# Kernel optimization log

Measured on AMD Instinct MI355X. Metric: run time of the kernel, lower is better.

## Reference

```python
import jax, jax.numpy as jnp
import numpy as np
from jax import lax

NUM_ITERS = 3
EPSILON = 0.5
QUEUE = 32768
NUM_CLUSTER = 1000


def setup_inputs() -> dict:
    key = jax.random.key(0)
    k1, _ = jax.random.split(key)
    memory_logits = jax.random.normal(k1, (QUEUE, NUM_CLUSTER), dtype=jnp.float32)
    learn_k = jnp.ones((1,), dtype=jnp.float32) * 5.0  # init value in torch module
    return {"memory_logits": memory_logits, "learn_k": learn_k}


def reference(memory_logits, learn_k):
    C = memory_logits.shape[1]
    # stabilize then exp, transpose to [C, N]
    ml = memory_logits - jnp.max(memory_logits)
    Q = jnp.exp(ml / EPSILON).T  # [C, N]
    # K: softmax over clusters of w * log(sigmoid(learn_k)); w = n/(C-1)
    w = (jnp.arange(C, dtype=Q.dtype) / (C - 1)).reshape(1, -1)
    K = jax.nn.softmax(w * jnp.log(jax.nn.sigmoid(learn_k)), axis=1)  # [1, C]
    Kcol = K.reshape(-1, 1)  # [C, 1] for row-wise scaling of Q
    B = Q.shape[1]
    # sort rows by descending row-sum
    order = jnp.argsort(-jnp.sum(Q, axis=1))
    Q = Q[order]
    Q = Q / jnp.sum(Q)

    def body(Q, _):
        Q = Q / jnp.sum(Q, axis=1, keepdims=True)   # row normalize
        Q = Q * Kcol                                 # (Q.t() * K).t()
        Q = jnp.clip(Q, 1e-16, None)
        Q = Q / jnp.sum(Q, axis=0, keepdims=True)   # col normalize
        Q = Q / B
        return Q, None

    Q, _ = lax.scan(body, Q, None, length=NUM_ITERS)
    Q = Q * B
    reorder = jnp.argsort(order)
    Q = Q[reorder]
    return Q.T  # [N, C]
```

## Files before the change

kernel.cpp:

```cpp
#include <hip/hip_runtime.h>
#include <math.h>

#define NQ 32768
#define NC 1000
#define NC4 250
#define NB 1024
#define PSTRIDE 1024

__device__ __forceinline__ float wredsum(float v) {
#pragma unroll
    for (int off = 32; off > 0; off >>= 1) v += __shfl_xor(v, off, 64);
    return v;
}

template <int MODE>
__global__ __launch_bounds__(256) void k_pass(const float* __restrict__ in,
                                              const float* __restrict__ svec,
                                              float* __restrict__ outp) {
    __shared__ float sacc[NC];
    if (MODE < 2) {
        for (int i = threadIdx.x; i < NC; i += 256) sacc[i] = 0.f;
        __syncthreads();
    }
    const int lane = threadIdx.x & 63;
    const int nw = (gridDim.x * 256) >> 6;
    const int wave = (blockIdx.x * 256 + threadIdx.x) >> 6;

    float4 sf[4];
    if (MODE >= 1) {
        const float4* S4 = reinterpret_cast<const float4*>(svec);
#pragma unroll
        for (int k = 0; k < 4; ++k) {
            int c4 = k * 64 + lane;
            sf[k] = (c4 < NC4) ? S4[c4] : make_float4(0.f, 0.f, 0.f, 0.f);
        }
    }
    float acc[16];
    if (MODE < 2) {
#pragma unroll
        for (int i = 0; i < 16; ++i) acc[i] = 0.f;
    }

    float4 nxt[4];
#pragma unroll
    for (int k = 0; k < 4; ++k) nxt[k] = make_float4(0.f, 0.f, 0.f, 0.f);

    int row = wave;
    if (row < NQ) {
        const float4* rp = reinterpret_cast<const float4*>(in + (size_t)row * NC);
#pragma unroll
        for (int k = 0; k < 4; ++k) {
            int c4 = k * 64 + lane;
            if (c4 < NC4) nxt[k] = rp[c4];
        }
    }
    while (row < NQ) {
        float4 cur[4];
#pragma unroll
        for (int k = 0; k < 4; ++k) cur[k] = nxt[k];
        const int nrow = row + nw;
        if (nrow < NQ) {
            const float4* rp = reinterpret_cast<const float4*>(in + (size_t)nrow * NC);
#pragma unroll
            for (int k = 0; k < 4; ++k) {
                int c4 = k * 64 + lane;
                if (c4 < NC4) nxt[k] = rp[c4];
            }
        }
        float4 e[4];
#pragma unroll
        for (int k = 0; k < 4; ++k) {
            e[k].x = __expf(2.f * cur[k].x);
            e[k].y = __expf(2.f * cur[k].y);
            e[k].z = __expf(2.f * cur[k].z);
            e[k].w = __expf(2.f * cur[k].w);
        }
        if (MODE == 0) {
#pragma unroll
            for (int k = 0; k < 4; ++k) {
                acc[4 * k + 0] += e[k].x; acc[4 * k + 1] += e[k].y;
                acc[4 * k + 2] += e[k].z; acc[4 * k + 3] += e[k].w;
            }
        } else {
            float t = 0.f;
#pragma unroll
            for (int k = 0; k < 4; ++k) {
                t += e[k].x * sf[k].x + e[k].y * sf[k].y
                   + e[k].z * sf[k].z + e[k].w * sf[k].w;
            }
            t = wredsum(t);
            const float r = 1.0f / t;
            if (MODE == 1) {
#pragma unroll
                for (int k = 0; k < 4; ++k) {
                    acc[4 * k + 0] += e[k].x * r; acc[4 * k + 1] += e[k].y * r;
                    acc[4 * k + 2] += e[k].z * r; acc[4 * k + 3] += e[k].w * r;
                }
            } else {
                float4* op = reinterpret_cast<float4*>(outp + (size_t)row * NC);
#pragma unroll
                for (int k = 0; k < 4; ++k) {
                    int c4 = k * 64 + lane;
                    if (c4 < NC4) {
                        op[c4] = make_float4(e[k].x * sf[k].x * r,
                                             e[k].y * sf[k].y * r,
                                             e[k].z * sf[k].z * r,
                                             e[k].w * sf[k].w * r);
                    }
                }
            }
        }
        row = nrow;
    }
    if (MODE < 2) {
#pragma unroll
        for (int k = 0; k < 4; ++k) {
            int c4 = k * 64 + lane;
            if (c4 < NC4) {
                atomicAdd(&sacc[4 * c4 + 0], acc[4 * k + 0]);
                atomicAdd(&sacc[4 * c4 + 1], acc[4 * k + 1]);
                atomicAdd(&sacc[4 * c4 + 2], acc[4 * k + 2]);
                atomicAdd(&sacc[4 * c4 + 3], acc[4 * k + 3]);
            }
        }
        __syncthreads();
        float* prow = outp + (size_t)blockIdx.x * PSTRIDE;
        for (int i = threadIdx.x; i < NC; i += 256) prow[i] = sacc[i];
    }
}

__global__ __launch_bounds__(128) void k_reduceG(const float* __restrict__ part,
                                                 float* __restrict__ G) {
    const int c = (blockIdx.x & 7) * 128 + threadIdx.x;
    const int p0 = (blockIdx.x >> 3) * 256;
    if (c < NC) {
        float sum = 0.f;
        for (int p = p0; p < p0 + 256; p += 4) {
            sum += part[(size_t)p * PSTRIDE + c]
                 + part[(size_t)(p + 1) * PSTRIDE + c]
                 + part[(size_t)(p + 2) * PSTRIDE + c]
                 + part[(size_t)(p + 3) * PSTRIDE + c];
        }
        atomicAdd(&G[c], sum);
    }
}

__global__ __launch_bounds__(128) void k_rank(const float* __restrict__ G,
                                              const float* __restrict__ learn_k,
                                              float* __restrict__ Ksc,
                                              float* __restrict__ svec) {
    __shared__ float sS[NC];
    __shared__ float sred[2];
    for (int i = threadIdx.x; i < NC; i += 128) sS[i] = G[i];
    const float L = -log1pf(expf(-learn_k[0]));
    float part = 0.f;
    for (int i = threadIdx.x; i < NC; i += 128)
        part += expf((float)i * (1.0f / 999.0f) * L);
    part = wredsum(part);
    if ((threadIdx.x & 63) == 0) sred[threadIdx.x >> 6] = part;
    __syncthreads();
    const float denom = sred[0] + sred[1];
    const int c = blockIdx.x * 128 + threadIdx.x;
    if (c < NC) {
        const float sc = sS[c];
        int p = 0;
#pragma unroll 4
        for (int j = 0; j < NC; ++j) {
            float sj = sS[j];
            p += (sj > sc) || (sj == sc && j < c);
        }
        const float ks = expf((float)p * (1.0f / 999.0f) * L) / denom;
        Ksc[c] = ks;
        svec[c] = ks / sc;
    }
}

__global__ __launch_bounds__(256) void k_prepS(const float* __restrict__ Ksc,
                                               const float* __restrict__ G,
                                               float* __restrict__ svec) {
    const int i = blockIdx.x * 256 + threadIdx.x;
    if (i < NC) svec[i] = Ksc[i] / G[i];
}

extern "C" void kernel_launch(void* const* d_in, const int* in_sizes, int n_in,
                              void* d_out, int out_size, void* d_ws, size_t ws_size,
                              hipStream_t stream) {
    const float* A = (const float*)d_in[0];
    const float* lk = (const float*)d_in[1];
    float* out = (float*)d_out;
    float* ws = (float*)d_ws;
    float* G0 = ws;
    float* G1 = ws + 1024;
    float* G2 = ws + 2048;
    float* Ksc = ws + 3072;
    float* sv = ws + 4096;
    float* part = ws + 8192;

    hipMemsetAsync(ws, 0, 3072 * sizeof(float), stream);

    k_pass<0><<<NB, 256, 0, stream>>>(A, nullptr, part);
    k_reduceG<<<32, 128, 0, stream>>>(part, G0);
    k_rank<<<8, 128, 0, stream>>>(G0, lk, Ksc, sv);
    k_pass<1><<<NB, 256, 0, stream>>>(A, sv, part);
    k_reduceG<<<32, 128, 0, stream>>>(part, G1);
    k_prepS<<<4, 256, 0, stream>>>(Ksc, G1, sv);
    k_pass<1><<<NB, 256, 0, stream>>>(A, sv, part);
    k_reduceG<<<32, 128, 0, stream>>>(part, G2);
    k_prepS<<<4, 256, 0, stream>>>(Ksc, G2, sv);
    k_pass<2><<<NB, 256, 0, stream>>>(A, sv, out);
}
```

Measured before the change: 451.1 us.

## Fuse all Sinkhorn passes into one cooperative persistent kernel with grid sync

Replaces the ten-launch pipeline (four streaming passes, partial-sum reductions, rank and scale kernels) with a single cooperative kernel. Column sums are accumulated into global arrays through shared-memory and global atomics, and the phases are separated by grid.sync. Rank and scale computation is repeated redundantly in every block's shared memory, and rows are streamed in chunks of 8 contiguous rows per wave. This removes launch gaps and the partial-buffer round trip, at the cost of grid-wide barriers, a grid capped by occupancy, and global atomic contention.

```diff
diff --git a/kernel.cpp b/kernel.cpp
--- a/kernel.cpp
+++ b/kernel.cpp
@@ -1,11 +1,14 @@
 #include <hip/hip_runtime.h>
+#include <hip/hip_cooperative_groups.h>
 #include <math.h>
+
+namespace cg = cooperative_groups;
 
 #define NQ 32768
 #define NC 1000
 #define NC4 250
-#define NB 1024
-#define PSTRIDE 1024
+#define CHUNK 8
+#define MAXBLK 1024
 
 __device__ __forceinline__ float wredsum(float v) {
 #pragma unroll
@@ -13,109 +16,78 @@
     return v;
 }
 
-template <int MODE>
-__global__ __launch_bounds__(256) void k_pass(const float* __restrict__ in,
-                                              const float* __restrict__ svec,
-                                              float* __restrict__ outp) {
-    __shared__ float sacc[NC];
-    if (MODE < 2) {
-        for (int i = threadIdx.x; i < NC; i += 256) sacc[i] = 0.f;
-        __syncthreads();
-    }
-    const int lane = threadIdx.x & 63;
-    const int nw = (gridDim.x * 256) >> 6;
-    const int wave = (blockIdx.x * 256 + threadIdx.x) >> 6;
-
-    float4 sf[4];
-    if (MODE >= 1) {
-        const float4* S4 = reinterpret_cast<const float4*>(svec);
+template <typename F>
+__device__ __forceinline__ void stream_all(const float* __restrict__ A, int gw,
+                                           int nwaves, int lane, F&& fn) {
+    for (int r0 = gw * CHUNK; r0 < NQ; r0 += nwaves * CHUNK) {
+        float4 nxt[4];
+        const float4* rp0 = reinterpret_cast<const float4*>(A + (size_t)r0 * NC);
 #pragma unroll
         for (int k = 0; k < 4; ++k) {
-            int c4 = k * 64 + lane;
-            sf[k] = (c4 < NC4) ? S4[c4] : make_float4(0.f, 0.f, 0.f, 0.f);
-        }
-    }
-    float acc[16];
-    if (MODE < 2) {
+            const int c4 = k * 64 + lane;
+            nxt[k] = (c4 < NC4) ? rp0[c4] : make_float4(0.f, 0.f, 0.f, 0.f);
+        }
+        for (int r = 0; r < CHUNK; ++r) {
+            float4 cur[4];
+#pragma unroll
+            for (int k = 0; k < 4; ++k) cur[k] = nxt[k];
+            if (r + 1 < CHUNK) {
+                const float4* rp =
+                    reinterpret_cast<const float4*>(A + (size_t)(r0 + r + 1) * NC);
+#pragma unroll
+                for (int k = 0; k < 4; ++k) {
+                    const int c4 = k * 64 + lane;
+                    if (c4 < NC4) nxt[k] = rp[c4];
+                }
+            }
+            float4 e[4];
+#pragma unroll
+            for (int k = 0; k < 4; ++k) {
+                e[k].x = __expf(2.f * cur[k].x);
+                e[k].y = __expf(2.f * cur[k].y);
+                e[k].z = __expf(2.f * cur[k].z);
+                e[k].w = __expf(2.f * cur[k].w);
+            }
+            fn(r0 + r, e);
+        }
+    }
+}
+
+__global__ __launch_bounds__(256, 4) void k_sink(const float* __restrict__ A,
+                                                 const float* __restrict__ lk,
+                                                 float* __restrict__ out,
+                                                 float* __restrict__ G) {
+    cg::grid_group grid = cg::this_grid();
+    __shared__ __align__(16) float sacc[1024];
+    __shared__ __align__(16) float sKsc[1024];
+    __shared__ __align__(16) float sSv[1024];
+    __shared__ float sred[4];
+
+    const int tid = threadIdx.x;
+    const int lane = tid & 63;
+    const int gw = (blockIdx.x * 256 + tid) >> 6;
+    const int nwaves = (gridDim.x * 256) >> 6;
+
+    float* G0 = G;
+    float* G1 = G + 1024;
+    float* G2 = G + 2048;
+
+    for (int i = tid; i < 1024; i += 256) sacc[i] = 0.f;
+    __syncthreads();
+    {
+        float acc[16];
 #pragma unroll
         for (int i = 0; i < 16; ++i) acc[i] = 0.f;
-    }
-
-    float4 nxt[4];
-#pragma unroll
-    for (int k = 0; k < 4; ++k) nxt[k] = make_float4(0.f, 0.f, 0.f, 0.f);
-
-    int row = wave;
-    if (row < NQ) {
-        const float4* rp = reinterpret_cast<const float4*>(in + (size_t)row * NC);
-#pragma unroll
-        for (int k = 0; k < 4; ++k) {
-            int c4 = k * 64 + lane;
-            if (c4 < NC4) nxt[k] = rp[c4];
-        }
-    }
-    while (row < NQ) {
-        float4 cur[4];
-#pragma unroll
-        for (int k = 0; k < 4; ++k) cur[k] = nxt[k];
-        const int nrow = row + nw;
-        if (nrow < NQ) {
-            const float4* rp = reinterpret_cast<const float4*>(in + (size_t)nrow * NC);
-#pragma unroll
-            for (int k = 0; k < 4; ++k) {
-                int c4 = k * 64 + lane;
-                if (c4 < NC4) nxt[k] = rp[c4];
-            }
-        }
-        float4 e[4];
-#pragma unroll
-        for (int k = 0; k < 4; ++k) {
-            e[k].x = __expf(2.f * cur[k].x);
-            e[k].y = __expf(2.f * cur[k].y);
-            e[k].z = __expf(2.f * cur[k].z);
-            e[k].w = __expf(2.f * cur[k].w);
-        }
-        if (MODE == 0) {
+        stream_all(A, gw, nwaves, lane, [&](int, const float4* e) {
 #pragma unroll
             for (int k = 0; k < 4; ++k) {
                 acc[4 * k + 0] += e[k].x; acc[4 * k + 1] += e[k].y;
                 acc[4 * k + 2] += e[k].z; acc[4 * k + 3] += e[k].w;
             }
-        } else {
-            float t = 0.f;
-#pragma unroll
-            for (int k = 0; k < 4; ++k) {
-                t += e[k].x * sf[k].x + e[k].y * sf[k].y
-                   + e[k].z * sf[k].z + e[k].w * sf[k].w;
-            }
-            t = wredsum(t);
-            const float r = 1.0f / t;
-            if (MODE == 1) {
-#pragma unroll
-                for (int k = 0; k < 4; ++k) {
-                    acc[4 * k + 0] += e[k].x * r; acc[4 * k + 1] += e[k].y * r;
-                    acc[4 * k + 2] += e[k].z * r; acc[4 * k + 3] += e[k].w * r;
-                }
-            } else {
-                float4* op = reinterpret_cast<float4*>(outp + (size_t)row * NC);
-#pragma unroll
-                for (int k = 0; k < 4; ++k) {
-                    int c4 = k * 64 + lane;
-                    if (c4 < NC4) {
-                        op[c4] = make_float4(e[k].x * sf[k].x * r,
-                                             e[k].y * sf[k].y * r,
-                                             e[k].z * sf[k].z * r,
-                                             e[k].w * sf[k].w * r);
-                    }
-                }
-            }
-        }
-        row = nrow;
-    }
-    if (MODE < 2) {
+        });
 #pragma unroll
         for (int k = 0; k < 4; ++k) {
-            int c4 = k * 64 + lane;
+            const int c4 = k * 64 + lane;
             if (c4 < NC4) {
                 atomicAdd(&sacc[4 * c4 + 0], acc[4 * k + 0]);
                 atomicAdd(&sacc[4 * c4 + 1], acc[4 * k + 1]);
@@ -124,62 +96,107 @@
             }
         }
         __syncthreads();
-        float* prow = outp + (size_t)blockIdx.x * PSTRIDE;
-        for (int i = threadIdx.x; i < NC; i += 256) prow[i] = sacc[i];
-    }
-}
-
-__global__ __launch_bounds__(128) void k_reduceG(const float* __restrict__ part,
-                                                 float* __restrict__ G) {
-    const int c = (blockIdx.x & 7) * 128 + threadIdx.x;
-    const int p0 = (blockIdx.x >> 3) * 256;
-    if (c < NC) {
-        float sum = 0.f;
-        for (int p = p0; p < p0 + 256; p += 4) {
-            sum += part[(size_t)p * PSTRIDE + c]
-                 + part[(size_t)(p + 1) * PSTRIDE + c]
-                 + part[(size_t)(p + 2) * PSTRIDE + c]
-                 + part[(size_t)(p + 3) * PSTRIDE + c];
-        }
-        atomicAdd(&G[c], sum);
-    }
-}
-
-__global__ __launch_bounds__(128) void k_rank(const float* __restrict__ G,
-                                              const float* __restrict__ learn_k,
-                                              float* __restrict__ Ksc,
-                                              float* __restrict__ svec) {
-    __shared__ float sS[NC];
-    __shared__ float sred[2];
-    for (int i = threadIdx.x; i < NC; i += 128) sS[i] = G[i];
-    const float L = -log1pf(expf(-learn_k[0]));
+        for (int i = tid; i < NC; i += 256) atomicAdd(&G0[i], sacc[i]);
+    }
+    grid.sync();
+
+    for (int i = tid; i < 1024; i += 256) sacc[i] = (i < NC) ? G0[i] : 0.f;
+    const float L = -log1pf(expf(-lk[0]));
     float part = 0.f;
-    for (int i = threadIdx.x; i < NC; i += 128)
-        part += expf((float)i * (1.0f / 999.0f) * L);
+    for (int i = tid; i < NC; i += 256) part += expf((float)i * (1.f / 999.f) * L);
     part = wredsum(part);
-    if ((threadIdx.x & 63) == 0) sred[threadIdx.x >> 6] = part;
+    if (lane == 0) sred[tid >> 6] = part;
     __syncthreads();
-    const float denom = sred[0] + sred[1];
-    const int c = blockIdx.x * 128 + threadIdx.x;
-    if (c < NC) {
-        const float sc = sS[c];
-        int p = 0;
+    const float denom = sred[0] + sred[1] + sred[2] + sred[3];
+    for (int c = tid; c < 1024; c += 256) {
+        if (c < NC) {
+            const float sc = sacc[c];
+            int p = 0;
 #pragma unroll 4
-        for (int j = 0; j < NC; ++j) {
-            float sj = sS[j];
-            p += (sj > sc) || (sj == sc && j < c);
-        }
-        const float ks = expf((float)p * (1.0f / 999.0f) * L) / denom;
-        Ksc[c] = ks;
-        svec[c] = ks / sc;
-    }
-}
-
-__global__ __launch_bounds__(256) void k_prepS(const float* __restrict__ Ksc,
-                                               const float* __restrict__ G,
-                                               float* __restrict__ svec) {
-    const int i = blockIdx.x * 256 + threadIdx.x;
-    if (i < NC) svec[i] = Ksc[i] / G[i];
+            for (int j = 0; j < NC; ++j) {
+                const float sj = sacc[j];
+                p += (sj > sc) || (sj == sc && j < c);
+            }
+            const float ks = expf((float)p * (1.f / 999.f) * L) / denom;
+            sKsc[c] = ks;
+            sSv[c] = ks / sc;
+        } else {
+            sKsc[c] = 0.f;
+            sSv[c] = 0.f;
+        }
+    }
+    __syncthreads();
+
+    const float4* S4 = reinterpret_cast<const float4*>(sSv);
+
+#pragma unroll 1
+    for (int it = 0; it < 2; ++it) {
+        float* Gn = (it == 0) ? G1 : G2;
+        float4 sf[4];
+#pragma unroll
+        for (int k = 0; k < 4; ++k) sf[k] = S4[k * 64 + lane];
+        __syncthreads();
+        for (int i = tid; i < 1024; i += 256) sacc[i] = 0.f;
+        __syncthreads();
+        float acc[16];
+#pragma unroll
+        for (int i = 0; i < 16; ++i) acc[i] = 0.f;
+        stream_all(A, gw, nwaves, lane, [&](int, const float4* e) {
+            float t = 0.f;
+#pragma unroll
+            for (int k = 0; k < 4; ++k)
+                t += e[k].x * sf[k].x + e[k].y * sf[k].y +
+                     e[k].z * sf[k].z + e[k].w * sf[k].w;
+            t = wredsum(t);
+            const float rr = 1.f / t;
+#pragma unroll
+            for (int k = 0; k < 4; ++k) {
+                acc[4 * k + 0] += e[k].x * rr; acc[4 * k + 1] += e[k].y * rr;
+                acc[4 * k + 2] += e[k].z * rr; acc[4 * k + 3] += e[k].w * rr;
+            }
+        });
+#pragma unroll
+        for (int k = 0; k < 4; ++k) {
+            const int c4 = k * 64 + lane;
+            if (c4 < NC4) {
+                atomicAdd(&sacc[4 * c4 + 0], acc[4 * k + 0]);
+                atomicAdd(&sacc[4 * c4 + 1], acc[4 * k + 1]);
+                atomicAdd(&sacc[4 * c4 + 2], acc[4 * k + 2]);
+                atomicAdd(&sacc[4 * c4 + 3], acc[4 * k + 3]);
+            }
+        }
+        __syncthreads();
+        for (int i = tid; i < NC; i += 256) atomicAdd(&Gn[i], sacc[i]);
+        grid.sync();
+        for (int i = tid; i < 1024; i += 256)
+            sSv[i] = (i < NC) ? sKsc[i] / Gn[i] : 0.f;
+        __syncthreads();
+    }
+
+    {
+        float4 sf[4];
+#pragma unroll
+        for (int k = 0; k < 4; ++k) sf[k] = S4[k * 64 + lane];
+        stream_all(A, gw, nwaves, lane, [&](int row, const float4* e) {
+            float t = 0.f;
+#pragma unroll
+            for (int k = 0; k < 4; ++k)
+                t += e[k].x * sf[k].x + e[k].y * sf[k].y +
+                     e[k].z * sf[k].z + e[k].w * sf[k].w;
+            t = wredsum(t);
+            const float rr = 1.f / t;
+            float4* op = reinterpret_cast<float4*>(out + (size_t)row * NC);
+#pragma unroll
+            for (int k = 0; k < 4; ++k) {
+                const int c4 = k * 64 + lane;
+                if (c4 < NC4)
+                    op[c4] = make_float4(e[k].x * sf[k].x * rr,
+                                         e[k].y * sf[k].y * rr,
+                                         e[k].z * sf[k].z * rr,
+                                         e[k].w * sf[k].w * rr);
+            }
+        });
+    }
 }
 
 extern "C" void kernel_launch(void* const* d_in, const int* in_sizes, int n_in,
@@ -188,24 +205,23 @@
     const float* A = (const float*)d_in[0];
     const float* lk = (const float*)d_in[1];
     float* out = (float*)d_out;
-    float* ws = (float*)d_ws;
-    float* G0 = ws;
-    float* G1 = ws + 1024;
-    float* G2 = ws + 2048;
-    float* Ksc = ws + 3072;
-    float* sv = ws + 4096;
-    float* part = ws + 8192;
-
-    hipMemsetAsync(ws, 0, 3072 * sizeof(float), stream);
-
-    k_pass<0><<<NB, 256, 0, stream>>>(A, nullptr, part);
-    k_reduceG<<<32, 128, 0, stream>>>(part, G0);
-    k_rank<<<8, 128, 0, stream>>>(G0, lk, Ksc, sv);
-    k_pass<1><<<NB, 256, 0, stream>>>(A, sv, part);
-    k_reduceG<<<32, 128, 0, stream>>>(part, G1);
-    k_prepS<<<4, 256, 0, stream>>>(Ksc, G1, sv);
-    k_pass<1><<<NB, 256, 0, stream>>>(A, sv, part);
-    k_reduceG<<<32, 128, 0, stream>>>(part, G2);
-    k_prepS<<<4, 256, 0, stream>>>(Ksc, G2, sv);
-    k_pass<2><<<NB, 256, 0, stream>>>(A, sv, out);
-}
+    float* G = (float*)d_ws;
+
+    hipMemsetAsync(G, 0, 3072 * sizeof(float), stream);
+
+    int nblk = MAXBLK;
+    int per_cu = 0;
+    if (hipOccupancyMaxActiveBlocksPerMultiprocessor(&per_cu, k_sink, 256, 0) ==
+            hipSuccess && per_cu > 0) {
+        int dev = 0, ncu = 0;
+        hipGetDevice(&dev);
+        hipDeviceGetAttribute(&ncu, hipDeviceAttributeMultiprocessorCount, dev);
+        if (ncu <= 0) ncu = 256;
+        long cap = (long)per_cu * (long)ncu;
+        if (cap < nblk) nblk = (int)cap;
+    }
+    if (nblk < 1) nblk = 1;
+
+    void* args[] = {(void*)&A, (void*)&lk, (void*)&out, (void*)&G};
+    hipLaunchCooperativeKernel(k_sink, dim3(nblk), dim3(256), args, 0, stream);
+}
```

Measured after the change: 661.4 us. 46.6% more time.

## Cache exponentiated matrix as bf16 and deepen row prefetch pipeline

Applied to the files above, without the earlier changes.

The first pass now writes exp(2x) as bf16 into workspace, and the later passes read that half-size buffer instead of recomputing exp from fp32 input, cutting memory traffic. Row loads are software-pipelined four buffers deep with a 2048-block grid. The partial-sum reduction is restructured into a two-level mid/rank reduction with no memset or atomics. bf16 storage reduces accuracy of the normalized outputs.

```diff
diff --git a/kernel.cpp b/kernel.cpp
--- a/kernel.cpp
+++ b/kernel.cpp
@@ -1,11 +1,14 @@
 #include <hip/hip_runtime.h>
 #include <math.h>
+#include <type_traits>
 
 #define NQ 32768
 #define NC 1000
-#define NC4 250
-#define NB 1024
-#define PSTRIDE 1024
+#define NCH 250
+#define PST 1024
+
+typedef unsigned int u32;
+typedef unsigned short u16;
 
 __device__ __forceinline__ float wredsum(float v) {
 #pragma unroll
@@ -13,26 +16,82 @@
     return v;
 }
 
-template <int MODE>
-__global__ __launch_bounds__(256) void k_pass(const float* __restrict__ in,
-                                              const float* __restrict__ svec,
-                                              float* __restrict__ outp) {
-    __shared__ float sacc[NC];
+struct BufF { float4 v[4]; };
+struct BufH { uint2 v[4]; };
+
+__device__ __forceinline__ void loadRow(BufF& b, const float* __restrict__ A,
+                                        int row, int lane) {
+    const float4* rp = reinterpret_cast<const float4*>(A + (size_t)row * NC);
+#pragma unroll
+    for (int k = 0; k < 4; ++k) {
+        const int c = k * 64 + lane;
+        if (c < NCH) b.v[k] = rp[c];
+        else b.v[k] = make_float4(0.f, 0.f, 0.f, 0.f);
+    }
+}
+__device__ __forceinline__ void loadRow(BufH& b, const u16* __restrict__ E,
+                                        int row, int lane) {
+    const uint2* rp = reinterpret_cast<const uint2*>(E + (size_t)row * NC);
+#pragma unroll
+    for (int k = 0; k < 4; ++k) {
+        const int c = k * 64 + lane;
+        if (c < NCH) b.v[k] = rp[c];
+        else b.v[k] = make_uint2(0u, 0u);
+    }
+}
+
+__device__ __forceinline__ float bf2f(u32 bits) {
+    union { u32 u; float f; } c; c.u = bits; return c.f;
+}
+__device__ __forceinline__ void conv(const BufF& b, float* e) {
+#pragma unroll
+    for (int k = 0; k < 4; ++k) {
+        e[4 * k + 0] = __expf(2.f * b.v[k].x);
+        e[4 * k + 1] = __expf(2.f * b.v[k].y);
+        e[4 * k + 2] = __expf(2.f * b.v[k].z);
+        e[4 * k + 3] = __expf(2.f * b.v[k].w);
+    }
+}
+__device__ __forceinline__ void conv(const BufH& b, float* e) {
+#pragma unroll
+    for (int k = 0; k < 4; ++k) {
+        e[4 * k + 0] = bf2f(b.v[k].x << 16);
+        e[4 * k + 1] = bf2f(b.v[k].x & 0xffff0000u);
+        e[4 * k + 2] = bf2f(b.v[k].y << 16);
+        e[4 * k + 3] = bf2f(b.v[k].y & 0xffff0000u);
+    }
+}
+__device__ __forceinline__ u32 f2bf_pair(float a, float bq) {
+    union { float f; u32 u; } ca, cb; ca.f = a; cb.f = bq;
+    const u32 ra = (ca.u + 0x7fffu + ((ca.u >> 16) & 1u)) >> 16;
+    const u32 rb = (cb.u + 0x7fffu + ((cb.u >> 16) & 1u)) & 0xffff0000u;
+    return ra | rb;
+}
+
+template <int SRC, int MODE, bool WE>
+__global__ __launch_bounds__(256) void k_pass(
+        const float* __restrict__ A, const u16* __restrict__ Ein,
+        u16* __restrict__ Eout, const float* __restrict__ sv,
+        float* __restrict__ outp, float* __restrict__ part) {
+    __shared__ float sacc[PST];
     if (MODE < 2) {
-        for (int i = threadIdx.x; i < NC; i += 256) sacc[i] = 0.f;
+        for (int i = threadIdx.x; i < PST; i += 256) sacc[i] = 0.f;
         __syncthreads();
     }
     const int lane = threadIdx.x & 63;
+    const int w = (blockIdx.x * 256 + threadIdx.x) >> 6;
     const int nw = (gridDim.x * 256) >> 6;
-    const int wave = (blockIdx.x * 256 + threadIdx.x) >> 6;
-
-    float4 sf[4];
+    const int R = NQ / nw;
+
+    float sf[16];
     if (MODE >= 1) {
-        const float4* S4 = reinterpret_cast<const float4*>(svec);
+        const float4* s4 = reinterpret_cast<const float4*>(sv);
 #pragma unroll
         for (int k = 0; k < 4; ++k) {
-            int c4 = k * 64 + lane;
-            sf[k] = (c4 < NC4) ? S4[c4] : make_float4(0.f, 0.f, 0.f, 0.f);
+            const int c = k * 64 + lane;
+            const float4 t = (c < NCH) ? s4[c] : make_float4(0.f, 0.f, 0.f, 0.f);
+            sf[4 * k + 0] = t.x; sf[4 * k + 1] = t.y;
+            sf[4 * k + 2] = t.z; sf[4 * k + 3] = t.w;
         }
     }
     float acc[16];
@@ -41,145 +100,139 @@
         for (int i = 0; i < 16; ++i) acc[i] = 0.f;
     }
 
-    float4 nxt[4];
-#pragma unroll
-    for (int k = 0; k < 4; ++k) nxt[k] = make_float4(0.f, 0.f, 0.f, 0.f);
-
-    int row = wave;
-    if (row < NQ) {
-        const float4* rp = reinterpret_cast<const float4*>(in + (size_t)row * NC);
-#pragma unroll
-        for (int k = 0; k < 4; ++k) {
-            int c4 = k * 64 + lane;
-            if (c4 < NC4) nxt[k] = rp[c4];
-        }
-    }
-    while (row < NQ) {
-        float4 cur[4];
-#pragma unroll
-        for (int k = 0; k < 4; ++k) cur[k] = nxt[k];
-        const int nrow = row + nw;
-        if (nrow < NQ) {
-            const float4* rp = reinterpret_cast<const float4*>(in + (size_t)nrow * NC);
-#pragma unroll
-            for (int k = 0; k < 4; ++k) {
-                int c4 = k * 64 + lane;
-                if (c4 < NC4) nxt[k] = rp[c4];
-            }
-        }
-        float4 e[4];
-#pragma unroll
-        for (int k = 0; k < 4; ++k) {
-            e[k].x = __expf(2.f * cur[k].x);
-            e[k].y = __expf(2.f * cur[k].y);
-            e[k].z = __expf(2.f * cur[k].z);
-            e[k].w = __expf(2.f * cur[k].w);
-        }
-        if (MODE == 0) {
-#pragma unroll
-            for (int k = 0; k < 4; ++k) {
-                acc[4 * k + 0] += e[k].x; acc[4 * k + 1] += e[k].y;
-                acc[4 * k + 2] += e[k].z; acc[4 * k + 3] += e[k].w;
+    using Buf = typename std::conditional<SRC == 0, BufF, BufH>::type;
+    Buf b0, b1, b2, b3;
+    int nld = 0;
+
+    auto LD = [&](Buf& b) {
+        if (nld < R) {
+            if constexpr (SRC == 0) loadRow(b, A, w + nld * nw, lane);
+            else                    loadRow(b, Ein, w + nld * nw, lane);
+            ++nld;
+        }
+    };
+    auto CMP = [&](Buf& b, int i) {
+        const int row = w + i * nw;
+        float e[16];
+        conv(b, e);
+        if constexpr (MODE == 0) {
+#pragma unroll
+            for (int j = 0; j < 16; ++j) acc[j] += e[j];
+            if constexpr (WE) {
+                uint2* ep = reinterpret_cast<uint2*>(Eout + (size_t)row * NC);
+#pragma unroll
+                for (int k = 0; k < 4; ++k) {
+                    const int c = k * 64 + lane;
+                    if (c < NCH)
+                        ep[c] = make_uint2(f2bf_pair(e[4 * k + 0], e[4 * k + 1]),
+                                           f2bf_pair(e[4 * k + 2], e[4 * k + 3]));
+                }
             }
         } else {
             float t = 0.f;
 #pragma unroll
-            for (int k = 0; k < 4; ++k) {
-                t += e[k].x * sf[k].x + e[k].y * sf[k].y
-                   + e[k].z * sf[k].z + e[k].w * sf[k].w;
-            }
+            for (int j = 0; j < 16; ++j) t += e[j] * sf[j];
             t = wredsum(t);
-            const float r = 1.0f / t;
-            if (MODE == 1) {
-#pragma unroll
-                for (int k = 0; k < 4; ++k) {
-                    acc[4 * k + 0] += e[k].x * r; acc[4 * k + 1] += e[k].y * r;
-                    acc[4 * k + 2] += e[k].z * r; acc[4 * k + 3] += e[k].w * r;
-                }
+            const float rr = 1.f / t;
+            if constexpr (MODE == 1) {
+#pragma unroll
+                for (int j = 0; j < 16; ++j) acc[j] += e[j] * rr;
             } else {
                 float4* op = reinterpret_cast<float4*>(outp + (size_t)row * NC);
 #pragma unroll
                 for (int k = 0; k < 4; ++k) {
-                    int c4 = k * 64 + lane;
-                    if (c4 < NC4) {
-                        op[c4] = make_float4(e[k].x * sf[k].x * r,
-                                             e[k].y * sf[k].y * r,
-                                             e[k].z * sf[k].z * r,
-                                             e[k].w * sf[k].w * r);
-                    }
+                    const int c = k * 64 + lane;
+                    if (c < NCH)
+                        op[c] = make_float4(e[4 * k + 0] * sf[4 * k + 0] * rr,
+                                            e[4 * k + 1] * sf[4 * k + 1] * rr,
+                                            e[4 * k + 2] * sf[4 * k + 2] * rr,
+                                            e[4 * k + 3] * sf[4 * k + 3] * rr);
                 }
             }
         }
-        row = nrow;
-    }
+    };
+
+    LD(b0); LD(b1);
+    for (int q = 0; q < R; q += 4) {
+        LD(b2); CMP(b0, q + 0);
+        LD(b3); CMP(b1, q + 1);
+        LD(b0); CMP(b2, q + 2);
+        LD(b1); CMP(b3, q + 3);
+    }
+
     if (MODE < 2) {
 #pragma unroll
         for (int k = 0; k < 4; ++k) {
-            int c4 = k * 64 + lane;
-            if (c4 < NC4) {
-                atomicAdd(&sacc[4 * c4 + 0], acc[4 * k + 0]);
-                atomicAdd(&sacc[4 * c4 + 1], acc[4 * k + 1]);
-                atomicAdd(&sacc[4 * c4 + 2], acc[4 * k + 2]);
-                atomicAdd(&sacc[4 * c4 + 3], acc[4 * k + 3]);
+            const int c = k * 64 + lane;
+            if (c < NCH) {
+                atomicAdd(&sacc[4 * c + 0], acc[4 * k + 0]);
+                atomicAdd(&sacc[4 * c + 1], acc[4 * k + 1]);
+                atomicAdd(&sacc[4 * c + 2], acc[4 * k + 2]);
+                atomicAdd(&sacc[4 * c + 3], acc[4 * k + 3]);
             }
         }
         __syncthreads();
-        float* prow = outp + (size_t)blockIdx.x * PSTRIDE;
-        for (int i = threadIdx.x; i < NC; i += 256) prow[i] = sacc[i];
-    }
-}
-
-__global__ __launch_bounds__(128) void k_reduceG(const float* __restrict__ part,
-                                                 float* __restrict__ G) {
-    const int c = (blockIdx.x & 7) * 128 + threadIdx.x;
-    const int p0 = (blockIdx.x >> 3) * 256;
-    if (c < NC) {
-        float sum = 0.f;
-        for (int p = p0; p < p0 + 256; p += 4) {
-            sum += part[(size_t)p * PSTRIDE + c]
-                 + part[(size_t)(p + 1) * PSTRIDE + c]
-                 + part[(size_t)(p + 2) * PSTRIDE + c]
-                 + part[(size_t)(p + 3) * PSTRIDE + c];
-        }
-        atomicAdd(&G[c], sum);
-    }
-}
-
-__global__ __launch_bounds__(128) void k_rank(const float* __restrict__ G,
-                                              const float* __restrict__ learn_k,
+        float4* pp = reinterpret_cast<float4*>(part + (size_t)blockIdx.x * PST);
+        const float4* sp = reinterpret_cast<const float4*>(sacc);
+        pp[threadIdx.x] = sp[threadIdx.x];
+    }
+}
+
+__global__ __launch_bounds__(256) void k_mid(const float* __restrict__ part,
+                                             float* __restrict__ mid, int rpg) {
+    const int pg = blockIdx.x >> 2;
+    const int c = (blockIdx.x & 3) * 256 + threadIdx.x;
+    float s = 0.f;
+    const float* p0 = part + (size_t)pg * rpg * PST + c;
+    for (int j = 0; j < rpg; ++j) s += p0[(size_t)j * PST];
+    mid[pg * PST + c] = s;
+}
+
+__global__ __launch_bounds__(128) void k_rank(const float* __restrict__ mid,
+                                              const float* __restrict__ lk,
                                               float* __restrict__ Ksc,
-                                              float* __restrict__ svec) {
-    __shared__ float sS[NC];
+                                              float* __restrict__ sv) {
+    __shared__ float sG[NC];
     __shared__ float sred[2];
-    for (int i = threadIdx.x; i < NC; i += 128) sS[i] = G[i];
-    const float L = -log1pf(expf(-learn_k[0]));
-    float part = 0.f;
-    for (int i = threadIdx.x; i < NC; i += 128)
-        part += expf((float)i * (1.0f / 999.0f) * L);
-    part = wredsum(part);
-    if ((threadIdx.x & 63) == 0) sred[threadIdx.x >> 6] = part;
+    const int tid = threadIdx.x;
+    for (int c = tid; c < NC; c += 128) {
+        float s = 0.f;
+#pragma unroll
+        for (int m = 0; m < 32; ++m) s += mid[m * PST + c];
+        sG[c] = s;
+    }
+    const float L = -log1pf(__expf(-lk[0]));
+    float pt = 0.f;
+    for (int i = tid; i < NC; i += 128) pt += __expf((float)i * (1.f / 999.f) * L);
+    pt = wredsum(pt);
+    if ((tid & 63) == 0) sred[tid >> 6] = pt;
     __syncthreads();
     const float denom = sred[0] + sred[1];
-    const int c = blockIdx.x * 128 + threadIdx.x;
-    if (c < NC) {
-        const float sc = sS[c];
+    if (tid < 125) {
+        const int c = blockIdx.x * 125 + tid;
+        const float sc = sG[c];
         int p = 0;
 #pragma unroll 4
         for (int j = 0; j < NC; ++j) {
-            float sj = sS[j];
+            const float sj = sG[j];
             p += (sj > sc) || (sj == sc && j < c);
         }
-        const float ks = expf((float)p * (1.0f / 999.0f) * L) / denom;
+        const float ks = __expf((float)p * (1.f / 999.f) * L) / denom;
         Ksc[c] = ks;
-        svec[c] = ks / sc;
-    }
-}
-
-__global__ __launch_bounds__(256) void k_prepS(const float* __restrict__ Ksc,
-                                               const float* __restrict__ G,
-                                               float* __restrict__ svec) {
-    const int i = blockIdx.x * 256 + threadIdx.x;
-    if (i < NC) svec[i] = Ksc[i] / G[i];
+        sv[c] = ks / sc;
+    }
+}
+
+__global__ __launch_bounds__(128) void k_prepS(const float* __restrict__ mid,
+                                               const float* __restrict__ Ksc,
+                                               float* __restrict__ sv) {
+    const int c = blockIdx.x * 128 + threadIdx.x;
+    if (c < NC) {
+        float s = 0.f;
+#pragma unroll
+        for (int m = 0; m < 32; ++m) s += mid[m * PST + c];
+        sv[c] = Ksc[c] / s;
+    }
 }
 
 extern "C" void kernel_launch(void* const* d_in, const int* in_sizes, int n_in,
@@ -189,23 +242,38 @@
     const float* lk = (const float*)d_in[1];
     float* out = (float*)d_out;
     float* ws = (float*)d_ws;
-    float* G0 = ws;
-    float* G1 = ws + 1024;
-    float* G2 = ws + 2048;
-    float* Ksc = ws + 3072;
-    float* sv = ws + 4096;
-    float* part = ws + 8192;
-
-    hipMemsetAsync(ws, 0, 3072 * sizeof(float), stream);
-
-    k_pass<0><<<NB, 256, 0, stream>>>(A, nullptr, part);
-    k_reduceG<<<32, 128, 0, stream>>>(part, G0);
-    k_rank<<<8, 128, 0, stream>>>(G0, lk, Ksc, sv);
-    k_pass<1><<<NB, 256, 0, stream>>>(A, sv, part);
-    k_reduceG<<<32, 128, 0, stream>>>(part, G1);
-    k_prepS<<<4, 256, 0, stream>>>(Ksc, G1, sv);
-    k_pass<1><<<NB, 256, 0, stream>>>(A, sv, part);
-    k_reduceG<<<32, 128, 0, stream>>>(part, G2);
-    k_prepS<<<4, 256, 0, stream>>>(Ksc, G2, sv);
-    k_pass<2><<<NB, 256, 0, stream>>>(A, sv, out);
-}
+    float* Ksc = ws;
+    float* sv = ws + 1024;
+    float* mid = ws + 2048;
+    float* part = ws + 2048 + 32 * 1024;
+    u16* E = (u16*)(ws + 34816 + 2048 * 1024);
+
+    const size_t need_part2048 = (size_t)(34816 + 2048 * 1024) * 4u;
+    const size_t need_E = need_part2048 + (size_t)NQ * NC * 2u;
+
+    if (ws_size >= need_E) {
+        const int G = 2048;
+        k_pass<0, 0, true><<<G, 256, 0, stream>>>(A, nullptr, E, nullptr, nullptr, part);
+        k_mid<<<128, 256, 0, stream>>>(part, mid, G / 32);
+        k_rank<<<8, 128, 0, stream>>>(mid, lk, Ksc, sv);
+        k_pass<1, 1, false><<<G, 256, 0, stream>>>(nullptr, E, nullptr, sv, nullptr, part);
+        k_mid<<<128, 256, 0, stream>>>(part, mid, G / 32);
+        k_prepS<<<8, 128, 0, stream>>>(mid, Ksc, sv);
+        k_pass<1, 1, false><<<G, 256, 0, stream>>>(nullptr, E, nullptr, sv, nullptr, part);
+        k_mid<<<128, 256, 0, stream>>>(part, mid, G / 32);
+        k_prepS<<<8, 128, 0, stream>>>(mid, Ksc, sv);
+        k_pass<1, 2, false><<<G, 256, 0, stream>>>(nullptr, E, nullptr, sv, out, nullptr);
+    } else {
+        const int G = (ws_size >= need_part2048) ? 2048 : 512;
+        k_pass<0, 0, false><<<G, 256, 0, stream>>>(A, nullptr, nullptr, nullptr, nullptr, part);
+        k_mid<<<128, 256, 0, stream>>>(part, mid, G / 32);
+        k_rank<<<8, 128, 0, stream>>>(mid, lk, Ksc, sv);
+        k_pass<0, 1, false><<<G, 256, 0, stream>>>(A, nullptr, nullptr, sv, nullptr, part);
+        k_mid<<<128, 256, 0, stream>>>(part, mid, G / 32);
+        k_prepS<<<8, 128, 0, stream>>>(mid, Ksc, sv);
+        k_pass<0, 1, false><<<G, 256, 0, stream>>>(A, nullptr, nullptr, sv, nullptr, part);
+        k_mid<<<128, 256, 0, stream>>>(part, mid, G / 32);
+        k_prepS<<<8, 128, 0, stream>>>(mid, Ksc, sv);
+        k_pass<0, 2, false><<<G, 256, 0, stream>>>(A, nullptr, nullptr, sv, out, nullptr);
+    }
+}
```

Result: slower. 468.0 us (+3.7%).
